# Kernel optimization log

Hardware: AMD Instinct MI355X
Metric: run time of the kernel (lower is better)

Reference implementation:

```python
import jax, jax.numpy as jnp
import numpy as np

NEG_SLOPE = 0.2  # PyG GATConv default negative_slope


def _gat(x, W, a_src, a_dst, b):
    # x: [G, N, F] -- G independent cliques of N nodes (full attention incl. self-loop,
    # matching PyG GATConv on the clique edge_index after remove+add self loops).
    G, N, F = x.shape
    H, D = a_src.shape
    h = jnp.einsum('gnf,fhd->gnhd', x, W.reshape(F, H, D))          # per-node linear, per head
    s_src = jnp.einsum('gnhd,hd->gnh', h, a_src)                     # alpha_src (source term)
    s_dst = jnp.einsum('gnhd,hd->gnh', h, a_dst)                     # alpha_dst (target term)
    # e[g,i,j,h]: edge j->i score = LeakyReLU(src_j + dst_i)
    e = jax.nn.leaky_relu(s_dst[:, :, None, :] + s_src[:, None, :, :], NEG_SLOPE)
    alpha = jax.nn.softmax(e, axis=2)                                # softmax over source j per target i
    out = jnp.einsum('gijh,gjhd->gihd', alpha, h)                    # aggregate messages
    return out.reshape(G, N, H * D) + b                              # concat heads + bias


def setup_inputs() -> dict:
    key = jax.random.key(0)
    ks = jax.random.split(key, 16)
    B, R, C, ENC = 4, 4096, 32, 15
    IN, HID, H, OUT, PROTO = 16, 32, 4, 6, 64
    s = 0.1
    return {
        'batch_xs': jax.random.normal(ks[0], (B, R, C), jnp.float32),
        'batch_pos_enc': jax.random.normal(ks[1], (B, C, ENC), jnp.float32),
        'W1': jax.random.normal(ks[2], (IN, H * HID), jnp.float32) * s,
        'a_src1': jax.random.normal(ks[3], (H, HID), jnp.float32) * s,
        'a_dst1': jax.random.normal(ks[4], (H, HID), jnp.float32) * s,
        'b1': jax.random.normal(ks[5], (H * HID,), jnp.float32) * s,
        'W2': jax.random.normal(ks[6], (H * HID, H * HID), jnp.float32) * s,
        'a_src2': jax.random.normal(ks[7], (H, HID), jnp.float32) * s,
        'a_dst2': jax.random.normal(ks[8], (H, HID), jnp.float32) * s,
        'b2': jax.random.normal(ks[9], (H * HID,), jnp.float32) * s,
        'W3': jax.random.normal(ks[10], (H * HID, H * OUT), jnp.float32) * s,
        'a_src3': jax.random.normal(ks[11], (H, OUT), jnp.float32) * s,
        'a_dst3': jax.random.normal(ks[12], (H, OUT), jnp.float32) * s,
        'b3': jax.random.normal(ks[13], (H * OUT,), jnp.float32) * s,
        'lin_w': jax.random.normal(ks[14], (H * OUT, PROTO), jnp.float32) * s,
        'lin_b': jax.random.normal(ks[15], (PROTO,), jnp.float32) * s,
    }


def reference(batch_xs, batch_pos_enc, W1, a_src1, a_dst1, b1, W2, a_src2, a_dst2, b2,
              W3, a_src3, a_dst3, b3, lin_w, lin_b):
    B, R, C = batch_xs.shape
    ENC = batch_pos_enc.shape[-1]
    # per-cell scalar feature + per-column positional encoding -> [B, R, C, 1+ENC]
    pe = jnp.broadcast_to(batch_pos_enc[:, None, :, :], (B, R, C, ENC))
    x = jnp.concatenate([batch_xs[..., None], pe], axis=-1)
    x = x.reshape(B * R, C, 1 + ENC)  # one clique graph per table row
    x = _gat(x, W1, a_src1, a_dst1, b1)
    x = _gat(x, W2, a_src2, a_dst2, b2)
    x = _gat(x, W3, a_src3, a_dst3, b3)   # [B*R, C, 24]
    x = x @ lin_w + lin_b                  # lin_1: 24 -> proto_dim
    x = x.mean(axis=1)                     # mean over N_col
    return x.reshape(B, R, -1)             # stacked per-batch outputs [B, N_row, proto_dim]
```

## Files before the change

### kernel.cpp

```cpp
#include <hip/hip_runtime.h>
#include <hip/hip_bf16.h>


typedef __attribute__((ext_vector_type(8))) short short8;
typedef __attribute__((ext_vector_type(4))) short short4v;
typedef __attribute__((ext_vector_type(4))) float f32x4;

#define MFMA16(a,b,c) __builtin_amdgcn_mfma_f32_16x16x32_bf16(a,b,c,0,0,0)
#define L2E 1.4426950408889634f

__device__ __forceinline__ short f2bf(float f) {
    __hip_bfloat16 h = __float2bfloat16(f);
    return *reinterpret_cast<short*>(&h);
}
__device__ __forceinline__ float fexp2(float x) { return __builtin_amdgcn_exp2f(x); }

__global__ __launch_bounds__(256) void build_wt(
    const float* __restrict__ W1, const float* __restrict__ as1, const float* __restrict__ ad1,
    const float* __restrict__ W2, const float* __restrict__ as2, const float* __restrict__ ad2,
    const float* __restrict__ W3, const float* __restrict__ as3, const float* __restrict__ ad3,
    short* __restrict__ ws)
{
    int i = blockIdx.x * 256 + threadIdx.x;
    float val = 0.f;
    if (i < 4608) {
        int n = i >> 5, k = i & 31;
        if (k < 16) {
            if (n < 128) val = W1[k*128 + n];
            else if (n < 136) {
                int cc = n - 128; const float* a = (cc < 4) ? as1 : ad1;
                for (int dl = 0; dl < 32; ++dl)
                    val += W1[k*128 + (cc&3)*32 + dl] * a[(cc&3)*32 + dl];
                val *= L2E;
            }
        }
        ws[i] = f2bf(val);
    } else if (i < 23040) {
        int j = i - 4608;
        int kq = j & 31, c = (j >> 5) & 15, kc = (j >> 9) & 3, nt = j >> 11;
        int n = nt*16 + c, k = kc*32 + kq;
        if (n < 128) val = W2[k*128 + n];
        else if (n < 136) {
            int cc = n - 128; const float* a = (cc < 4) ? as2 : ad2;
            for (int dl = 0; dl < 32; ++dl)
                val += W2[k*128 + (cc&3)*32 + dl] * a[(cc&3)*32 + dl];
            val *= L2E;
        }
        ws[i] = f2bf(val);
    } else {
        int j = i - 23040;
        int kq = j & 31, c = (j >> 5) & 15, kc = (j >> 9) & 3, nt = j >> 11;
        int n = nt*16 + c, k = kc*32 + kq;
        if (n < 24) val = W3[k*24 + n];
        else {
            int cc = n - 24; const float* a = (cc < 4) ? as3 : ad3;
            for (int dl = 0; dl < 6; ++dl)
                val += W3[k*24 + (cc&3)*6 + dl] * a[(cc&3)*6 + dl];
            val *= L2E;
        }
        ws[i] = f2bf(val);
    }
}


template<int KC, int NT, int NTH>
__device__ __forceinline__ void gemm_ht(short* buf, const short* __restrict__ wt,
                                        float* ss, int c, int q)
{
    const f32x4 zf = {0.f, 0.f, 0.f, 0.f};
    short8 afr[2][KC];
    #pragma unroll
    for (int mt = 0; mt < 2; ++mt)
      #pragma unroll
      for (int kc = 0; kc < KC; ++kc)
        afr[mt][kc] = *(const short8*)&buf[(mt*16 + c)*136 + kc*32 + q*8];
    int sw = c >> 1;
    #pragma unroll
    for (int nt = 0; nt < NT; ++nt) {
        f32x4 a0 = zf, a1 = zf;
        #pragma unroll
        for (int kc = 0; kc < KC; ++kc) {
            short8 bfr = *(const short8*)&wt[((nt*KC + kc)*16 + c)*32 + q*8];
            a0 = MFMA16(afr[0][kc], bfr, a0);
            a1 = MFMA16(afr[1][kc], bfr, a1);
        }
        if (nt < NTH) {
            int d = nt*16 + c;
            short4v h0, h1;
            #pragma unroll
            for (int r = 0; r < 4; ++r) { h0[r] = f2bf(a0[r]); h1[r] = f2bf(a1[r]); }
            *(short4v*)&buf[d*32 + (q ^ sw)*4]       = h0;
            *(short4v*)&buf[d*32 + ((4+q) ^ sw)*4]   = h1;
        } else if (c < 8) {
            *(f32x4*)&ss[c*32 + q*4]      = a0;
            *(f32x4*)&ss[c*32 + 16 + q*4] = a1;
        }
    }
}

__device__ __forceinline__ void agg12(const short* buf, const float* ss,
                                      int c, int q, f32x4 (&acc)[8][2], float (&rden)[4][2])
{
    const f32x4 zf = {0.f, 0.f, 0.f, 0.f};
    int sw = c >> 1;
    #pragma unroll
    for (int hd = 0; hd < 4; ++hd) {
        f32x4 v0 = *(const f32x4*)&ss[hd*32 + q*8];
        f32x4 v1 = *(const f32x4*)&ss[hd*32 + q*8 + 4];
        short8 pf[2];
        #pragma unroll
        for (int it = 0; it < 2; ++it) {
            float sd = ss[(4+hd)*32 + it*16 + c];
            float den = 0.f; short8 t;
            #pragma unroll
            for (int v = 0; v < 8; ++v) {
                float sj = (v < 4) ? v0[v] : v1[v-4];
                float e = sd + sj; e = fmaxf(e, 0.2f*e);
                float p = fexp2(e);
                den += p;
                t[v] = f2bf(p);
            }
            den += __shfl_xor(den, 16, 64);
            den += __shfl_xor(den, 32, 64);
            pf[it] = t; rden[hd][it] = 1.0f / den;
        }
        #pragma unroll
        for (int m2 = 0; m2 < 2; ++m2) {
            int mt = hd*2 + m2, d = mt*16 + c;
            short4v lo = *(const short4v*)&buf[d*32 + ((2*q)   ^ sw)*4];
            short4v hi = *(const short4v*)&buf[d*32 + ((2*q+1) ^ sw)*4];
            short8 af = __builtin_shufflevector(lo, hi, 0,1,2,3,4,5,6,7);
            acc[mt][0] = MFMA16(af, pf[0], zf);
            acc[mt][1] = MFMA16(af, pf[1], zf);
        }
    }
}

__device__ __forceinline__ void trans_phase(const f32x4 (&acc)[8][2], const float (&rden)[4][2],
                                            const float* bias, short* xb, int c, int q)
{
    #pragma unroll
    for (int mt = 0; mt < 8; ++mt) {
        f32x4 bv = *(const f32x4*)&bias[mt*16 + q*4];
        #pragma unroll
        for (int nt = 0; nt < 2; ++nt) {
            float rd = rden[mt >> 1][nt];
            int ii = nt*16 + c;
            short4v o;
            #pragma unroll
            for (int r = 0; r < 4; ++r) o[r] = f2bf(fmaf(acc[mt][nt][r], rd, bv[r]));
            *(short4v*)&xb[ii*136 + mt*16 + q*4] = o;
        }
    }
}

__device__ __forceinline__ void gemm3_ht(short* buf, const short* __restrict__ wt,
                                         float* ss, int c, int q, int lane)
{
    const f32x4 zf = {0.f, 0.f, 0.f, 0.f};
    short8 afr[2][4];
    #pragma unroll
    for (int mt = 0; mt < 2; ++mt)
      #pragma unroll
      for (int kc = 0; kc < 4; ++kc)
        afr[mt][kc] = *(const short8*)&buf[(mt*16 + c)*136 + kc*32 + q*8];
    {
        const short4v z4 = {0, 0, 0, 0};
        #pragma unroll
        for (int k = 0; k < 5; ++k) {
            int flat = lane + k*64;
            int z = flat >> 3, gg = flat & 7;
            int row = (z/10)*16 + 6 + (z%10);
            *(short4v*)&buf[row*32 + gg*4] = z4;
        }
    }
    #pragma unroll
    for (int nt = 0; nt < 2; ++nt) {
        f32x4 a0 = zf, a1 = zf;
        #pragma unroll
        for (int kc = 0; kc < 4; ++kc) {
            short8 bfr = *(const short8*)&wt[((nt*4 + kc)*16 + c)*32 + q*8];
            a0 = MFMA16(afr[0][kc], bfr, a0);
            a1 = MFMA16(afr[1][kc], bfr, a1);
        }
        int p = nt*16 + c;
        if (p < 24) {
            int row = (p/6)*16 + (p%6);
            int sw3 = (row & 15) >> 1;
            short4v h0, h1;
            #pragma unroll
            for (int r = 0; r < 4; ++r) { h0[r] = f2bf(a0[r]); h1[r] = f2bf(a1[r]); }
            *(short4v*)&buf[row*32 + (q ^ sw3)*4]     = h0;
            *(short4v*)&buf[row*32 + ((4+q) ^ sw3)*4] = h1;
        } else if (c >= 8) {
            *(f32x4*)&ss[(c-8)*32 + q*4]      = a0;
            *(f32x4*)&ss[(c-8)*32 + 16 + q*4] = a1;
        }
    }
}

__device__ __forceinline__ void agg3_mean(const short* buf, const float* ss,
                                          const float* b3, float* mcol, int c, int q)
{
    const f32x4 zf = {0.f, 0.f, 0.f, 0.f};
    int sw = c >> 1;
    float vout[4];
    #pragma unroll
    for (int hd = 0; hd < 4; ++hd) {
        f32x4 v0 = *(const f32x4*)&ss[hd*32 + q*8];
        f32x4 v1 = *(const f32x4*)&ss[hd*32 + q*8 + 4];
        short8 pf[2];
        #pragma unroll
        for (int it = 0; it < 2; ++it) {
            float sd = ss[(4+hd)*32 + it*16 + c];
            float pv[8]; float den = 0.f;
            #pragma unroll
            for (int v = 0; v < 8; ++v) {
                float sj = (v < 4) ? v0[v] : v1[v-4];
                float e = sd + sj; e = fmaxf(e, 0.2f*e);
                pv[v] = fexp2(e);
                den += pv[v];
            }
            den += __shfl_xor(den, 16, 64);
            den += __shfl_xor(den, 32, 64);
            float rd = 1.0f / den;
            short8 t;
            #pragma unroll
            for (int v = 0; v < 8; ++v) t[v] = f2bf(pv[v] * rd);
            pf[it] = t;
        }
        int d = hd*16 + c;
        short4v lo = *(const short4v*)&buf[d*32 + ((2*q)   ^ sw)*4];
        short4v hi = *(const short4v*)&buf[d*32 + ((2*q+1) ^ sw)*4];
        short8 bf_ = __builtin_shufflevector(lo, hi, 0,1,2,3,4,5,6,7);
        f32x4 o0 = MFMA16(pf[0], bf_, zf);
        f32x4 o1 = MFMA16(pf[1], bf_, zf);
        float s = (o0[0]+o0[1]) + (o0[2]+o0[3]) + (o1[0]+o1[1]) + (o1[2]+o1[3]);
        s += __shfl_xor(s, 16, 64);
        s += __shfl_xor(s, 32, 64);
        vout[hd] = s;
    }
    if (q == 0 && c < 6) {
        #pragma unroll
        for (int hd = 0; hd < 4; ++hd)
            mcol[hd*6 + c] = vout[hd] * (1.f/32.f) + b3[hd*6 + c];
    }
}

__global__ __launch_bounds__(256, 4) void gat_mfma(
    const float* __restrict__ xs, const float* __restrict__ pe,
    const short* __restrict__ ws,
    const float* __restrict__ b1, const float* __restrict__ b2, const float* __restrict__ b3,
    const float* __restrict__ LW, const float* __restrict__ lb,
    float* __restrict__ out, int R)
{
    __shared__ short buf[4][4352];
    __shared__ float ssx[4][256];

    int t = threadIdx.x;
    int w = t >> 6, lane = t & 63;
    int c = lane & 15, q = lane >> 4;
    int g = blockIdx.x * 4 + w;
    int b = g / R;

    short* xb = buf[w];
    float* ss = ssx[w];

    {
        int j = lane >> 1, half = lane & 1;
        float v[8];
        if (half == 0) {
            v[0] = xs[g*32 + j];
            #pragma unroll
            for (int kk = 0; kk < 7; ++kk) v[1+kk] = pe[b*480 + j*15 + kk];
        } else {
            #pragma unroll
            for (int kk = 0; kk < 8; ++kk) v[kk] = pe[b*480 + j*15 + 7 + kk];
        }
        short8 px;
        #pragma unroll
        for (int kk = 0; kk < 8; ++kk) px[kk] = f2bf(v[kk]);
        *(short8*)&xb[j*136 + half*8] = px;
        *(short8*)&xb[j*136 + 16 + half*8] = (short8){0,0,0,0,0,0,0,0};
    }

    const short* wt1 = ws;
    const short* wt2 = ws + 4608;
    const short* wt3 = ws + 23040;

    {
        gemm_ht<1,9,8>(xb, wt1, ss, c, q);
        f32x4 acc[8][2]; float rden[4][2];
        agg12(xb, ss, c, q, acc, rden);
        trans_phase(acc, rden, b1, xb, c, q);
    }
    {
        gemm_ht<4,9,8>(xb, wt2, ss, c, q);
        f32x4 acc[8][2]; float rden[4][2];
        agg12(xb, ss, c, q, acc, rden);
        trans_phase(acc, rden, b2, xb, c, q);
    }
    {
        gemm3_ht(xb, wt3, ss, c, q, lane);
        agg3_mean(xb, ss, b3, ss, c, q);
    }
    {
        float o = lb[lane];
        #pragma unroll
        for (int cc = 0; cc < 24; ++cc)
            o = fmaf(ss[cc], LW[cc*64 + lane], o);
        out[g*64 + lane] = o;
    }
}

extern "C" void kernel_launch(void* const* d_in, const int* in_sizes, int n_in,
                              void* d_out, int out_size, void* d_ws, size_t ws_size,
                              hipStream_t stream) {
    const float* xs  = (const float*)d_in[0];
    const float* pe  = (const float*)d_in[1];
    const float* W1  = (const float*)d_in[2];
    const float* as1 = (const float*)d_in[3];
    const float* ad1 = (const float*)d_in[4];
    const float* b1  = (const float*)d_in[5];
    const float* W2  = (const float*)d_in[6];
    const float* as2 = (const float*)d_in[7];
    const float* ad2 = (const float*)d_in[8];
    const float* b2  = (const float*)d_in[9];
    const float* W3  = (const float*)d_in[10];
    const float* as3 = (const float*)d_in[11];
    const float* ad3 = (const float*)d_in[12];
    const float* b3  = (const float*)d_in[13];
    const float* LW  = (const float*)d_in[14];
    const float* lb  = (const float*)d_in[15];
    float* o = (float*)d_out;
    short* ws = (short*)d_ws;

    int G = in_sizes[0] / 32;
    int B = in_sizes[1] / 480;
    int R = G / B;

    build_wt<<<dim3(106), dim3(256), 0, stream>>>(W1, as1, ad1, W2, as2, ad2,
                                                  W3, as3, ad3, ws);
    gat_mfma<<<dim3(G/4), dim3(256), 0, stream>>>(xs, pe, ws, b1, b2, b3, LW, lb, o, R);
}
```

Before: 96.45 us.

## Shrink per-wave LDS via split-half GEMM/aggregation and XOR-swizzled layout

Splits each GAT layer's projection and aggregation into two head-halves that reuse one smaller LDS region, holding the finished outputs in registers until both halves are done. It also packs the score buffer into the same per-wave LDS tile and replaces the padded row stride with an XOR swizzle. The goal is to cut LDS per block so that 5 blocks per CU fit instead of 4, with fewer bank conflicts. In exchange, register pressure rises from the pending outputs and aliasing the buffers makes correctness depend on the order of writes and reads within the wave.

```diff
diff --git a/kernel.cpp b/kernel.cpp
--- a/kernel.cpp
+++ b/kernel.cpp
@@ -8,6 +8,7 @@
 
 #define MFMA16(a,b,c) __builtin_amdgcn_mfma_f32_16x16x32_bf16(a,b,c,0,0,0)
 #define L2E 1.4426950408889634f
+#define MEMBAR() asm volatile("" ::: "memory")
 
 __device__ __forceinline__ short f2bf(float f) {
     __hip_bfloat16 h = __float2bfloat16(f);
@@ -63,20 +64,44 @@
 }
 
 
-template<int KC, int NT, int NTH>
-__device__ __forceinline__ void gemm_ht(short* buf, const short* __restrict__ wt,
-                                        float* ss, int c, int q)
-{
-    const f32x4 zf = {0.f, 0.f, 0.f, 0.f};
-    short8 afr[2][KC];
+template<int KC>
+__device__ __forceinline__ void preload_a(const short* xb, int c, int q, short8 (&afr)[2][KC])
+{
+    constexpr int MSK = (KC == 1) ? 3 : 7;
     #pragma unroll
     for (int mt = 0; mt < 2; ++mt)
       #pragma unroll
       for (int kc = 0; kc < KC; ++kc)
-        afr[mt][kc] = *(const short8*)&buf[(mt*16 + c)*136 + kc*32 + q*8];
+        afr[mt][kc] = *(const short8*)&xb[(mt*16 + c)*128 + ((kc*4 + q) ^ (c & MSK))*8];
+}
+
+template<int KC>
+__device__ __forceinline__ void score_col(const short8 (&afr)[2][KC], const short* __restrict__ wt,
+                                          float* ss, int c, int q)
+{
+    const f32x4 zf = {0.f, 0.f, 0.f, 0.f};
+    f32x4 a0 = zf, a1 = zf;
+    #pragma unroll
+    for (int kc = 0; kc < KC; ++kc) {
+        short8 bfr = *(const short8*)&wt[((8*KC + kc)*16 + c)*32 + q*8];
+        a0 = MFMA16(afr[0][kc], bfr, a0);
+        a1 = MFMA16(afr[1][kc], bfr, a1);
+    }
+    if (c < 8) {
+        *(f32x4*)&ss[c*32 + q*4]      = a0;
+        *(f32x4*)&ss[c*32 + 16 + q*4] = a1;
+    }
+}
+
+template<int KC>
+__device__ __forceinline__ void gemm_half(const short8 (&afr)[2][KC], const short* __restrict__ wt,
+                                          short* ht, int h, int c, int q)
+{
+    const f32x4 zf = {0.f, 0.f, 0.f, 0.f};
     int sw = c >> 1;
     #pragma unroll
-    for (int nt = 0; nt < NT; ++nt) {
+    for (int ntl = 0; ntl < 4; ++ntl) {
+        int nt = h*4 + ntl;
         f32x4 a0 = zf, a1 = zf;
         #pragma unroll
         for (int kc = 0; kc < KC; ++kc) {
@@ -84,27 +109,23 @@
             a0 = MFMA16(afr[0][kc], bfr, a0);
             a1 = MFMA16(afr[1][kc], bfr, a1);
         }
-        if (nt < NTH) {
-            int d = nt*16 + c;
-            short4v h0, h1;
-            #pragma unroll
-            for (int r = 0; r < 4; ++r) { h0[r] = f2bf(a0[r]); h1[r] = f2bf(a1[r]); }
-            *(short4v*)&buf[d*32 + (q ^ sw)*4]       = h0;
-            *(short4v*)&buf[d*32 + ((4+q) ^ sw)*4]   = h1;
-        } else if (c < 8) {
-            *(f32x4*)&ss[c*32 + q*4]      = a0;
-            *(f32x4*)&ss[c*32 + 16 + q*4] = a1;
-        }
-    }
-}
-
-__device__ __forceinline__ void agg12(const short* buf, const float* ss,
-                                      int c, int q, f32x4 (&acc)[8][2], float (&rden)[4][2])
+        short4v h0, h1;
+        #pragma unroll
+        for (int r = 0; r < 4; ++r) { h0[r] = f2bf(a0[r]); h1[r] = f2bf(a1[r]); }
+        int rl = ntl*16 + c;
+        *(short4v*)&ht[rl*32 + ((q ^ sw))*4]     = h0;
+        *(short4v*)&ht[rl*32 + (((4+q) ^ sw))*4] = h1;
+    }
+}
+
+__device__ __forceinline__ void agg_half(const short* ht, const float* ss, int h,
+                                         int c, int q, f32x4 (&acc)[4][2], float (&rdh)[2][2])
 {
     const f32x4 zf = {0.f, 0.f, 0.f, 0.f};
     int sw = c >> 1;
     #pragma unroll
-    for (int hd = 0; hd < 4; ++hd) {
+    for (int hh = 0; hh < 2; ++hh) {
+        int hd = h*2 + hh;
         f32x4 v0 = *(const f32x4*)&ss[hd*32 + q*8];
         f32x4 v1 = *(const f32x4*)&ss[hd*32 + q*8 + 4];
         short8 pf[2];
@@ -122,48 +143,85 @@
             }
             den += __shfl_xor(den, 16, 64);
             den += __shfl_xor(den, 32, 64);
-            pf[it] = t; rden[hd][it] = 1.0f / den;
+            pf[it] = t; rdh[hh][it] = 1.0f / den;
         }
         #pragma unroll
         for (int m2 = 0; m2 < 2; ++m2) {
-            int mt = hd*2 + m2, d = mt*16 + c;
-            short4v lo = *(const short4v*)&buf[d*32 + ((2*q)   ^ sw)*4];
-            short4v hi = *(const short4v*)&buf[d*32 + ((2*q+1) ^ sw)*4];
+            int mtl = hh*2 + m2, rl = mtl*16 + c;
+            short4v lo = *(const short4v*)&ht[rl*32 + ((2*q)   ^ sw)*4];
+            short4v hi = *(const short4v*)&ht[rl*32 + ((2*q+1) ^ sw)*4];
             short8 af = __builtin_shufflevector(lo, hi, 0,1,2,3,4,5,6,7);
-            acc[mt][0] = MFMA16(af, pf[0], zf);
-            acc[mt][1] = MFMA16(af, pf[1], zf);
-        }
-    }
-}
-
-__device__ __forceinline__ void trans_phase(const f32x4 (&acc)[8][2], const float (&rden)[4][2],
-                                            const float* bias, short* xb, int c, int q)
-{
-    #pragma unroll
-    for (int mt = 0; mt < 8; ++mt) {
+            acc[mtl][0] = MFMA16(af, pf[0], zf);
+            acc[mtl][1] = MFMA16(af, pf[1], zf);
+        }
+    }
+}
+
+__device__ __forceinline__ void finish_half(const f32x4 (&acc)[4][2], const float (&rdh)[2][2],
+                                            const float* bias, int h, int q, short4v (&pend)[4][2])
+{
+    #pragma unroll
+    for (int mtl = 0; mtl < 4; ++mtl) {
+        int mt = h*4 + mtl;
         f32x4 bv = *(const f32x4*)&bias[mt*16 + q*4];
         #pragma unroll
         for (int nt = 0; nt < 2; ++nt) {
-            float rd = rden[mt >> 1][nt];
+            float rd = rdh[mtl >> 1][nt];
+            short4v o;
+            #pragma unroll
+            for (int r = 0; r < 4; ++r) o[r] = f2bf(fmaf(acc[mtl][nt][r], rd, bv[r]));
+            pend[mtl][nt] = o;
+        }
+    }
+}
+
+__device__ __forceinline__ void write_xb(const short4v (&p0)[4][2], const short4v (&p1)[4][2],
+                                         short* xb, int c, int q)
+{
+    #pragma unroll
+    for (int h = 0; h < 2; ++h)
+      #pragma unroll
+      for (int mtl = 0; mtl < 4; ++mtl) {
+        int mt = h*4 + mtl;
+        #pragma unroll
+        for (int nt = 0; nt < 2; ++nt) {
             int ii = nt*16 + c;
-            short4v o;
-            #pragma unroll
-            for (int r = 0; r < 4; ++r) o[r] = f2bf(fmaf(acc[mt][nt][r], rd, bv[r]));
-            *(short4v*)&xb[ii*136 + mt*16 + q*4] = o;
-        }
-    }
-}
-
-__device__ __forceinline__ void gemm3_ht(short* buf, const short* __restrict__ wt,
-                                         float* ss, int c, int q, int lane)
+            short4v val = h ? p1[mtl][nt] : p0[mtl][nt];
+            *(short4v*)&xb[ii*128 + ((2*mt + (q>>1)) ^ (ii & 7))*8 + (q & 1)*4] = val;
+        }
+      }
+}
+
+template<int KC>
+__device__ __forceinline__ void layer12(short* buf, const short* __restrict__ wt,
+                                        const float* bias, int c, int q)
+{
+    float* ss = reinterpret_cast<float*>(buf + 2048);
+    short8 afr[2][KC];
+    preload_a<KC>(buf, c, q, afr);
+    MEMBAR();
+    score_col<KC>(afr, wt, ss, c, q);
+    f32x4 acc[4][2]; float rdh[2][2];
+    short4v pend0[4][2], pend1[4][2];
+    gemm_half<KC>(afr, wt, buf, 0, c, q);
+    agg_half(buf, ss, 0, c, q, acc, rdh);
+    finish_half(acc, rdh, bias, 0, q, pend0);
+    gemm_half<KC>(afr, wt, buf, 1, c, q);
+    agg_half(buf, ss, 1, c, q, acc, rdh);
+    finish_half(acc, rdh, bias, 1, q, pend1);
+    MEMBAR();
+    write_xb(pend0, pend1, buf, c, q);
+    MEMBAR();
+}
+
+__device__ __forceinline__ void layer3(short* buf, const short* __restrict__ wt,
+                                       const float* b3, int c, int q, int lane)
 {
     const f32x4 zf = {0.f, 0.f, 0.f, 0.f};
+    float* ss = reinterpret_cast<float*>(buf + 2048);
     short8 afr[2][4];
-    #pragma unroll
-    for (int mt = 0; mt < 2; ++mt)
-      #pragma unroll
-      for (int kc = 0; kc < 4; ++kc)
-        afr[mt][kc] = *(const short8*)&buf[(mt*16 + c)*136 + kc*32 + q*8];
+    preload_a<4>(buf, c, q, afr);
+    MEMBAR();
     {
         const short4v z4 = {0, 0, 0, 0};
         #pragma unroll
@@ -190,19 +248,14 @@
             short4v h0, h1;
             #pragma unroll
             for (int r = 0; r < 4; ++r) { h0[r] = f2bf(a0[r]); h1[r] = f2bf(a1[r]); }
-            *(short4v*)&buf[row*32 + (q ^ sw3)*4]     = h0;
-            *(short4v*)&buf[row*32 + ((4+q) ^ sw3)*4] = h1;
+            *(short4v*)&buf[row*32 + ((q ^ sw3))*4]     = h0;
+            *(short4v*)&buf[row*32 + (((4+q) ^ sw3))*4] = h1;
         } else if (c >= 8) {
             *(f32x4*)&ss[(c-8)*32 + q*4]      = a0;
             *(f32x4*)&ss[(c-8)*32 + 16 + q*4] = a1;
         }
     }
-}
-
-__device__ __forceinline__ void agg3_mean(const short* buf, const float* ss,
-                                          const float* b3, float* mcol, int c, int q)
-{
-    const f32x4 zf = {0.f, 0.f, 0.f, 0.f};
+    MEMBAR();
     int sw = c >> 1;
     float vout[4];
     #pragma unroll
@@ -229,9 +282,9 @@
             for (int v = 0; v < 8; ++v) t[v] = f2bf(pv[v] * rd);
             pf[it] = t;
         }
-        int d = hd*16 + c;
-        short4v lo = *(const short4v*)&buf[d*32 + ((2*q)   ^ sw)*4];
-        short4v hi = *(const short4v*)&buf[d*32 + ((2*q+1) ^ sw)*4];
+        int rl = hd*16 + c;
+        short4v lo = *(const short4v*)&buf[rl*32 + ((2*q)   ^ sw)*4];
+        short4v hi = *(const short4v*)&buf[rl*32 + ((2*q+1) ^ sw)*4];
         short8 bf_ = __builtin_shufflevector(lo, hi, 0,1,2,3,4,5,6,7);
         f32x4 o0 = MFMA16(pf[0], bf_, zf);
         f32x4 o1 = MFMA16(pf[1], bf_, zf);
@@ -240,22 +293,23 @@
         s += __shfl_xor(s, 32, 64);
         vout[hd] = s;
     }
+    MEMBAR();
     if (q == 0 && c < 6) {
         #pragma unroll
         for (int hd = 0; hd < 4; ++hd)
-            mcol[hd*6 + c] = vout[hd] * (1.f/32.f) + b3[hd*6 + c];
-    }
-}
-
-__global__ __launch_bounds__(256, 4) void gat_mfma(
+            ss[hd*6 + c] = vout[hd] * (1.f/32.f) + b3[hd*6 + c];
+    }
+    MEMBAR();
+}
+
+__global__ __launch_bounds__(256, 5) void gat_mfma(
     const float* __restrict__ xs, const float* __restrict__ pe,
     const short* __restrict__ ws,
     const float* __restrict__ b1, const float* __restrict__ b2, const float* __restrict__ b3,
     const float* __restrict__ LW, const float* __restrict__ lb,
     float* __restrict__ out, int R)
 {
-    __shared__ short buf[4][4352];
-    __shared__ float ssx[4][256];
+    __shared__ short buf[4][4096];
 
     int t = threadIdx.x;
     int w = t >> 6, lane = t & 63;
@@ -264,7 +318,6 @@
     int b = g / R;
 
     short* xb = buf[w];
-    float* ss = ssx[w];
 
     {
         int j = lane >> 1, half = lane & 1;
@@ -280,31 +333,22 @@
         short8 px;
         #pragma unroll
         for (int kk = 0; kk < 8; ++kk) px[kk] = f2bf(v[kk]);
-        *(short8*)&xb[j*136 + half*8] = px;
-        *(short8*)&xb[j*136 + 16 + half*8] = (short8){0,0,0,0,0,0,0,0};
-    }
+        int s3 = j & 3;
+        *(short8*)&xb[j*128 + (half ^ s3)*8]       = px;
+        *(short8*)&xb[j*128 + (((2+half) ^ s3))*8] = (short8){0,0,0,0,0,0,0,0};
+    }
+    MEMBAR();
 
     const short* wt1 = ws;
     const short* wt2 = ws + 4608;
     const short* wt3 = ws + 23040;
 
+    layer12<1>(xb, wt1, b1, c, q);
+    layer12<4>(xb, wt2, b2, c, q);
+    layer3(xb, wt3, b3, c, q, lane);
+
     {
-        gemm_ht<1,9,8>(xb, wt1, ss, c, q);
-        f32x4 acc[8][2]; float rden[4][2];
-        agg12(xb, ss, c, q, acc, rden);
-        trans_phase(acc, rden, b1, xb, c, q);
-    }
-    {
-        gemm_ht<4,9,8>(xb, wt2, ss, c, q);
-        f32x4 acc[8][2]; float rden[4][2];
-        agg12(xb, ss, c, q, acc, rden);
-        trans_phase(acc, rden, b2, xb, c, q);
-    }
-    {
-        gemm3_ht(xb, wt3, ss, c, q, lane);
-        agg3_mean(xb, ss, b3, ss, c, q);
-    }
-    {
+        const float* ss = reinterpret_cast<const float*>(xb + 2048);
         float o = lb[lane];
         #pragma unroll
         for (int cc = 0; cc < 24; ++cc)
```

Result: slower. 114.5 us (+18.7%).

## Split each graph across two wavefronts with block-level syncs

Applied to the files above, without the earlier changes.

Each 32-node clique graph is now processed by two cooperating wavefronts instead of one. The projection GEMM columns, the attention heads and the final output are split between them, with __syncthreads barriers between phases. Each block now handles two graphs, the grid doubles, and launch bounds rise to 8 blocks per CU. The aim is to cut per-wave register pressure, since the accumulator arrays shrink, and to raise parallelism. The cost is many block-wide barriers, one wave redundantly loading the full A fragments, and idle waves during input load and output.

```diff
diff --git a/kernel.cpp b/kernel.cpp
--- a/kernel.cpp
+++ b/kernel.cpp
@@ -63,20 +63,25 @@
 }
 
 
-template<int KC, int NT, int NTH>
-__device__ __forceinline__ void gemm_ht(short* buf, const short* __restrict__ wt,
-                                        float* ss, int c, int q)
-{
-    const f32x4 zf = {0.f, 0.f, 0.f, 0.f};
-    short8 afr[2][KC];
+template<int KC>
+__device__ __forceinline__ void preload_a(const short* xb, int c, int q, short8 (&afr)[2][KC])
+{
     #pragma unroll
     for (int mt = 0; mt < 2; ++mt)
       #pragma unroll
       for (int kc = 0; kc < KC; ++kc)
-        afr[mt][kc] = *(const short8*)&buf[(mt*16 + c)*136 + kc*32 + q*8];
+        afr[mt][kc] = *(const short8*)&xb[(mt*16 + c)*136 + kc*32 + q*8];
+}
+
+template<int KC>
+__device__ __forceinline__ void gemm_ht(const short8 (&afr)[2][KC], const short* __restrict__ wt,
+                                        short* buf, float* ss, int c, int q, int wl)
+{
+    const f32x4 zf = {0.f, 0.f, 0.f, 0.f};
     int sw = c >> 1;
     #pragma unroll
-    for (int nt = 0; nt < NT; ++nt) {
+    for (int ntl = 0; ntl < 4; ++ntl) {
+        int nt = wl*4 + ntl;
         f32x4 a0 = zf, a1 = zf;
         #pragma unroll
         for (int kc = 0; kc < KC; ++kc) {
@@ -84,30 +89,40 @@
             a0 = MFMA16(afr[0][kc], bfr, a0);
             a1 = MFMA16(afr[1][kc], bfr, a1);
         }
-        if (nt < NTH) {
-            int d = nt*16 + c;
-            short4v h0, h1;
-            #pragma unroll
-            for (int r = 0; r < 4; ++r) { h0[r] = f2bf(a0[r]); h1[r] = f2bf(a1[r]); }
-            *(short4v*)&buf[d*32 + (q ^ sw)*4]       = h0;
-            *(short4v*)&buf[d*32 + ((4+q) ^ sw)*4]   = h1;
-        } else if (c < 8) {
+        int d = nt*16 + c;
+        short4v h0, h1;
+        #pragma unroll
+        for (int r = 0; r < 4; ++r) { h0[r] = f2bf(a0[r]); h1[r] = f2bf(a1[r]); }
+        *(short4v*)&buf[d*32 + ((q ^ sw))*4]     = h0;
+        *(short4v*)&buf[d*32 + (((4+q) ^ sw))*4] = h1;
+    }
+    if (wl == 1) {
+        f32x4 a0 = zf, a1 = zf;
+        #pragma unroll
+        for (int kc = 0; kc < KC; ++kc) {
+            short8 bfr = *(const short8*)&wt[((8*KC + kc)*16 + c)*32 + q*8];
+            a0 = MFMA16(afr[0][kc], bfr, a0);
+            a1 = MFMA16(afr[1][kc], bfr, a1);
+        }
+        if (c < 8) {
             *(f32x4*)&ss[c*32 + q*4]      = a0;
             *(f32x4*)&ss[c*32 + 16 + q*4] = a1;
         }
     }
 }
 
-__device__ __forceinline__ void agg12(const short* buf, const float* ss,
-                                      int c, int q, f32x4 (&acc)[8][2], float (&rden)[4][2])
+__device__ __forceinline__ void agg_pend(const short* buf, const float* ss,
+                                         const float* bias, int c, int q, int wl,
+                                         short4v (&pend)[4][2])
 {
     const f32x4 zf = {0.f, 0.f, 0.f, 0.f};
     int sw = c >> 1;
     #pragma unroll
-    for (int hd = 0; hd < 4; ++hd) {
+    for (int hh = 0; hh < 2; ++hh) {
+        int hd = wl*2 + hh;
         f32x4 v0 = *(const f32x4*)&ss[hd*32 + q*8];
         f32x4 v1 = *(const f32x4*)&ss[hd*32 + q*8 + 4];
-        short8 pf[2];
+        short8 pf[2]; float rdh[2];
         #pragma unroll
         for (int it = 0; it < 2; ++it) {
             float sd = ss[(4+hd)*32 + it*16 + c];
@@ -122,60 +137,77 @@
             }
             den += __shfl_xor(den, 16, 64);
             den += __shfl_xor(den, 32, 64);
-            pf[it] = t; rden[hd][it] = 1.0f / den;
+            pf[it] = t; rdh[it] = 1.0f / den;
         }
         #pragma unroll
         for (int m2 = 0; m2 < 2; ++m2) {
-            int mt = hd*2 + m2, d = mt*16 + c;
+            int mtl = hh*2 + m2, mt = wl*4 + mtl, d = mt*16 + c;
             short4v lo = *(const short4v*)&buf[d*32 + ((2*q)   ^ sw)*4];
             short4v hi = *(const short4v*)&buf[d*32 + ((2*q+1) ^ sw)*4];
             short8 af = __builtin_shufflevector(lo, hi, 0,1,2,3,4,5,6,7);
-            acc[mt][0] = MFMA16(af, pf[0], zf);
-            acc[mt][1] = MFMA16(af, pf[1], zf);
-        }
-    }
-}
-
-__device__ __forceinline__ void trans_phase(const f32x4 (&acc)[8][2], const float (&rden)[4][2],
-                                            const float* bias, short* xb, int c, int q)
-{
-    #pragma unroll
-    for (int mt = 0; mt < 8; ++mt) {
-        f32x4 bv = *(const f32x4*)&bias[mt*16 + q*4];
-        #pragma unroll
-        for (int nt = 0; nt < 2; ++nt) {
-            float rd = rden[mt >> 1][nt];
-            int ii = nt*16 + c;
-            short4v o;
-            #pragma unroll
-            for (int r = 0; r < 4; ++r) o[r] = f2bf(fmaf(acc[mt][nt][r], rd, bv[r]));
-            *(short4v*)&xb[ii*136 + mt*16 + q*4] = o;
-        }
-    }
-}
-
-__device__ __forceinline__ void gemm3_ht(short* buf, const short* __restrict__ wt,
-                                         float* ss, int c, int q, int lane)
+            f32x4 bv = *(const f32x4*)&bias[mt*16 + q*4];
+            #pragma unroll
+            for (int it = 0; it < 2; ++it) {
+                f32x4 acc = MFMA16(af, pf[it], zf);
+                short4v o;
+                #pragma unroll
+                for (int r = 0; r < 4; ++r) o[r] = f2bf(fmaf(acc[r], rdh[it], bv[r]));
+                pend[mtl][it] = o;
+            }
+        }
+    }
+}
+
+__device__ __forceinline__ void write_xb(const short4v (&pend)[4][2], short* xb,
+                                         int c, int q, int wl)
+{
+    #pragma unroll
+    for (int mtl = 0; mtl < 4; ++mtl) {
+        int mt = wl*4 + mtl;
+        #pragma unroll
+        for (int it = 0; it < 2; ++it) {
+            int ii = it*16 + c;
+            *(short4v*)&xb[ii*136 + mt*16 + q*4] = pend[mtl][it];
+        }
+    }
+}
+
+template<int KC>
+__device__ __forceinline__ void layer12(short* buf, float* ss, const short* __restrict__ wt,
+                                        const float* bias, int c, int q, int wl)
+{
+    short8 afr[2][KC];
+    preload_a<KC>(buf, c, q, afr);
+    __syncthreads();
+    gemm_ht<KC>(afr, wt, buf, ss, c, q, wl);
+    __syncthreads();
+    short4v pend[4][2];
+    agg_pend(buf, ss, bias, c, q, wl, pend);
+    __syncthreads();
+    write_xb(pend, buf, c, q, wl);
+}
+
+__device__ __forceinline__ void layer3(short* buf, float* ss, const short* __restrict__ wt,
+                                       const float* b3, int c, int q, int lane, int wl)
 {
     const f32x4 zf = {0.f, 0.f, 0.f, 0.f};
     short8 afr[2][4];
-    #pragma unroll
-    for (int mt = 0; mt < 2; ++mt)
-      #pragma unroll
-      for (int kc = 0; kc < 4; ++kc)
-        afr[mt][kc] = *(const short8*)&buf[(mt*16 + c)*136 + kc*32 + q*8];
+    preload_a<4>(buf, c, q, afr);
+    __syncthreads();
     {
         const short4v z4 = {0, 0, 0, 0};
         #pragma unroll
-        for (int k = 0; k < 5; ++k) {
-            int flat = lane + k*64;
-            int z = flat >> 3, gg = flat & 7;
-            int row = (z/10)*16 + 6 + (z%10);
-            *(short4v*)&buf[row*32 + gg*4] = z4;
-        }
-    }
-    #pragma unroll
-    for (int nt = 0; nt < 2; ++nt) {
+        for (int k = 0; k < 3; ++k) {
+            int flat = (wl*64 + lane) + k*128;
+            if (flat < 320) {
+                int z = flat >> 3, gg = flat & 7;
+                int row = (z/10)*16 + 6 + (z%10);
+                *(short4v*)&buf[row*32 + gg*4] = z4;
+            }
+        }
+    }
+    {
+        int nt = wl;
         f32x4 a0 = zf, a1 = zf;
         #pragma unroll
         for (int kc = 0; kc < 4; ++kc) {
@@ -190,23 +222,19 @@
             short4v h0, h1;
             #pragma unroll
             for (int r = 0; r < 4; ++r) { h0[r] = f2bf(a0[r]); h1[r] = f2bf(a1[r]); }
-            *(short4v*)&buf[row*32 + (q ^ sw3)*4]     = h0;
-            *(short4v*)&buf[row*32 + ((4+q) ^ sw3)*4] = h1;
+            *(short4v*)&buf[row*32 + ((q ^ sw3))*4]     = h0;
+            *(short4v*)&buf[row*32 + (((4+q) ^ sw3))*4] = h1;
         } else if (c >= 8) {
             *(f32x4*)&ss[(c-8)*32 + q*4]      = a0;
             *(f32x4*)&ss[(c-8)*32 + 16 + q*4] = a1;
         }
     }
-}
-
-__device__ __forceinline__ void agg3_mean(const short* buf, const float* ss,
-                                          const float* b3, float* mcol, int c, int q)
-{
-    const f32x4 zf = {0.f, 0.f, 0.f, 0.f};
+    __syncthreads();
     int sw = c >> 1;
-    float vout[4];
-    #pragma unroll
-    for (int hd = 0; hd < 4; ++hd) {
+    float vout[2];
+    #pragma unroll
+    for (int hh = 0; hh < 2; ++hh) {
+        int hd = wl*2 + hh;
         f32x4 v0 = *(const f32x4*)&ss[hd*32 + q*8];
         f32x4 v1 = *(const f32x4*)&ss[hd*32 + q*8 + 4];
         short8 pf[2];
@@ -229,44 +257,47 @@
             for (int v = 0; v < 8; ++v) t[v] = f2bf(pv[v] * rd);
             pf[it] = t;
         }
-        int d = hd*16 + c;
-        short4v lo = *(const short4v*)&buf[d*32 + ((2*q)   ^ sw)*4];
-        short4v hi = *(const short4v*)&buf[d*32 + ((2*q+1) ^ sw)*4];
+        int rl = hd*16 + c;
+        short4v lo = *(const short4v*)&buf[rl*32 + ((2*q)   ^ sw)*4];
+        short4v hi = *(const short4v*)&buf[rl*32 + ((2*q+1) ^ sw)*4];
         short8 bf_ = __builtin_shufflevector(lo, hi, 0,1,2,3,4,5,6,7);
         f32x4 o0 = MFMA16(pf[0], bf_, zf);
         f32x4 o1 = MFMA16(pf[1], bf_, zf);
         float s = (o0[0]+o0[1]) + (o0[2]+o0[3]) + (o1[0]+o1[1]) + (o1[2]+o1[3]);
         s += __shfl_xor(s, 16, 64);
         s += __shfl_xor(s, 32, 64);
-        vout[hd] = s;
-    }
+        vout[hh] = s;
+    }
+    __syncthreads();
     if (q == 0 && c < 6) {
         #pragma unroll
-        for (int hd = 0; hd < 4; ++hd)
-            mcol[hd*6 + c] = vout[hd] * (1.f/32.f) + b3[hd*6 + c];
-    }
-}
-
-__global__ __launch_bounds__(256, 4) void gat_mfma(
+        for (int hh = 0; hh < 2; ++hh)
+            ss[(wl*2 + hh)*6 + c] = vout[hh] * (1.f/32.f) + b3[(wl*2 + hh)*6 + c];
+    }
+    __syncthreads();
+}
+
+__global__ __launch_bounds__(256, 8) void gat_mfma(
     const float* __restrict__ xs, const float* __restrict__ pe,
     const short* __restrict__ ws,
     const float* __restrict__ b1, const float* __restrict__ b2, const float* __restrict__ b3,
     const float* __restrict__ LW, const float* __restrict__ lb,
     float* __restrict__ out, int R)
 {
-    __shared__ short buf[4][4352];
-    __shared__ float ssx[4][256];
+    __shared__ short buf[2][4352];
+    __shared__ float ssx[2][256];
 
     int t = threadIdx.x;
     int w = t >> 6, lane = t & 63;
+    int gl = w >> 1, wl = w & 1;
     int c = lane & 15, q = lane >> 4;
-    int g = blockIdx.x * 4 + w;
+    int g = blockIdx.x * 2 + gl;
     int b = g / R;
 
-    short* xb = buf[w];
-    float* ss = ssx[w];
-
-    {
+    short* xb = buf[gl];
+    float* ss = ssx[gl];
+
+    if (wl == 0) {
         int j = lane >> 1, half = lane & 1;
         float v[8];
         if (half == 0) {
@@ -283,28 +314,19 @@
         *(short8*)&xb[j*136 + half*8] = px;
         *(short8*)&xb[j*136 + 16 + half*8] = (short8){0,0,0,0,0,0,0,0};
     }
+    __syncthreads();
 
     const short* wt1 = ws;
     const short* wt2 = ws + 4608;
     const short* wt3 = ws + 23040;
 
-    {
-        gemm_ht<1,9,8>(xb, wt1, ss, c, q);
-        f32x4 acc[8][2]; float rden[4][2];
-        agg12(xb, ss, c, q, acc, rden);
-        trans_phase(acc, rden, b1, xb, c, q);
-    }
-    {
-        gemm_ht<4,9,8>(xb, wt2, ss, c, q);
-        f32x4 acc[8][2]; float rden[4][2];
-        agg12(xb, ss, c, q, acc, rden);
-        trans_phase(acc, rden, b2, xb, c, q);
-    }
-    {
-        gemm3_ht(xb, wt3, ss, c, q, lane);
-        agg3_mean(xb, ss, b3, ss, c, q);
-    }
-    {
+    layer12<1>(xb, ss, wt1, b1, c, q, wl);
+    __syncthreads();
+    layer12<4>(xb, ss, wt2, b2, c, q, wl);
+    __syncthreads();
+    layer3(xb, ss, wt3, b3, c, q, lane, wl);
+
+    if (wl == 0) {
         float o = lb[lane];
         #pragma unroll
         for (int cc = 0; cc < 24; ++cc)
@@ -341,5 +363,5 @@
 
     build_wt<<<dim3(106), dim3(256), 0, stream>>>(W1, as1, ad1, W2, as2, ad2,
                                                   W3, as3, ad3, ws);
-    gat_mfma<<<dim3(G/4), dim3(256), 0, stream>>>(xs, pe, ws, b1, b2, b3, LW, lb, o, R);
-}
+    gat_mfma<<<dim3(G/2), dim3(256), 0, stream>>>(xs, pe, ws, b1, b2, b3, LW, lb, o, R);
+}
```

Measured after the change: 122.2 us. 26.8% more time.
